# Performance work log

Measured on AMD Instinct MI355X. Metric: run time of the kernel, lower is better.

Reference implementation:

```python
import jax, jax.numpy as jnp
import numpy as np

B, L, H = 4, 512, 768          # batch, seq_len, bert hidden
S, R = 100, 100                # num candidate spans, num relation pairs
E = 128                        # size embedding dim
TE, TR = 8, 6                  # entity / relation types
MAX_ENT_LEN = 100
NEG = -1e20


def _span_masks(rng, b, n, seq_len, max_len):
    # contiguous span masks with lengths in [1, max_len-1] so sum(-1) < max_len
    starts = rng.integers(0, seq_len - 1, size=(b, n))
    lengths = rng.integers(1, max_len, size=(b, n))
    ends = np.minimum(starts + lengths, seq_len)
    pos = np.arange(seq_len)
    m = (pos[None, None, :] >= starts[..., None]) & (pos[None, None, :] < ends[..., None])
    return jnp.asarray(m.astype(np.int32))


def setup_inputs() -> dict:
    rng = np.random.default_rng(0)
    key = jax.random.key(0)
    k = jax.random.split(key, 6)
    return {
        "last_hidden_state": jax.random.normal(k[0], (B, L, H), jnp.float32),
        "entity_mask": _span_masks(rng, B, S, L, MAX_ENT_LEN),
        "relations": jnp.asarray(rng.integers(0, S, size=(B, R, 2)).astype(np.int32)),
        "relation_context_mask": _span_masks(rng, B, R, L, MAX_ENT_LEN),
        "relation_sample_mask": jnp.asarray(rng.integers(0, 2, size=(B, R)).astype(np.int32)),
        "size_emb": jax.random.normal(k[1], (MAX_ENT_LEN, E), jnp.float32) * 0.02,
        "span_w": jax.random.normal(k[2], (E + 2 * H, TE), jnp.float32) * 0.02,
        "span_b": jnp.zeros((TE,), jnp.float32),
        "rel_w": jax.random.normal(k[3], (2 * E + 3 * H, TR), jnp.float32) * 0.02,
        "rel_b": jnp.zeros((TR,), jnp.float32),
    }


def _masked_max(h, mask):
    # h: [B,L,H], mask: [B,N,L] int {0,1} -> [B,N,H]
    mf = mask[..., None].astype(h.dtype)                       # [B,N,L,1]
    masked = jnp.where(mf == 0, jnp.asarray(NEG, h.dtype), h[:, None] * mf)
    return masked.max(axis=2)


def reference(last_hidden_state, entity_mask, relations, relation_context_mask,
              relation_sample_mask, size_emb, span_w, span_b, rel_w, rel_b):
    b = last_hidden_state.shape[0]
    # ---- entity classification ----
    context = last_hidden_state[:, 0]                          # CLS pooling [B,H]
    entity_size = size_emb[entity_mask.sum(-1)]                # [B,S,E]
    entity = _masked_max(last_hidden_state, entity_mask)       # [B,S,H]
    ctx = jnp.broadcast_to(context[:, None], (b, entity.shape[1], context.shape[-1]))
    entity_repr = jnp.concatenate([entity, ctx, entity_size], axis=-1)
    entity_logit = entity_repr @ span_w + span_b               # [B,S,TE]
    # ---- relation classification ----
    rel_ctx = _masked_max(last_hidden_state, relation_context_mask)  # [B,R,H]
    rel_ctx = jnp.where(relation_sample_mask[..., None] == 1,
                        jnp.zeros((), rel_ctx.dtype), rel_ctx)
    r = relations.shape[1]
    flat = relations.reshape(b, r * 2)                         # [B,2R]
    pair = jnp.take_along_axis(entity, flat[..., None], axis=1).reshape(b, r, -1)      # [B,R,2H]
    pair_size = jnp.take_along_axis(entity_size, flat[..., None], axis=1).reshape(b, r, -1)  # [B,R,2E]
    relation_repr = jnp.concatenate([rel_ctx, pair, pair_size], axis=-1)
    relation_logit = relation_repr @ rel_w + rel_b             # [B,R,TR]
    return entity_logit, relation_logit
```

## Files before the change

kernel.cpp:

```cpp
#include <hip/hip_runtime.h>

#define Bn 4
#define Ln 512
#define Hn 768
#define Sn 100
#define Rn 100
#define En 128
#define TEn 8
#define TRn 6
#define NEGF (-1e20f)
#define W 8
#define NBLK (Ln / W)
#define H4 (Hn / 4)
#define E4 (En / 4)
#define NTHR 640

__device__ __forceinline__ float4 fmax4(float4 a, float4 b) {
    return make_float4(fmaxf(a.x, b.x), fmaxf(a.y, b.y),
                       fmaxf(a.z, b.z), fmaxf(a.w, b.w));
}

__global__ void __launch_bounds__(192)
blockmax_kernel(const float* __restrict__ hid, float* __restrict__ bmax) {
    int bj = blockIdx.x;
    int b = bj / NBLK, j = bj % NBLK;
    int tid = threadIdx.x;
    const float4* src = (const float4*)(hid + ((size_t)b * Ln + j * W) * Hn);
    float4 m0 = src[tid];
    float4 m1 = src[(size_t)H4 + tid];
    #pragma unroll
    for (int r = 2; r < W; r += 2) {
        m0 = fmax4(m0, src[(size_t)r * H4 + tid]);
        m1 = fmax4(m1, src[(size_t)(r + 1) * H4 + tid]);
    }
    ((float4*)(bmax + (size_t)bj * Hn))[tid] = fmax4(m0, m1);
}

__device__ __forceinline__ void scan_span(const int* __restrict__ mask,
                                          int lane, int* start, int* end) {
    const int4* m4 = (const int4*)(mask + lane * 8);
    int4 a = m4[0], c = m4[1];
    int mm[8] = {a.x, a.y, a.z, a.w, c.x, c.y, c.z, c.w};
    int first = 0x7fffffff, last = -1;
    #pragma unroll
    for (int r = 0; r < 8; ++r) {
        if (mm[r] != 0) {
            int row = lane * 8 + r;
            first = min(first, row);
            last = max(last, row);
        }
    }
    #pragma unroll
    for (int off = 1; off < 64; off <<= 1) {
        first = min(first, __shfl_xor(first, off, 64));
        last = max(last, __shfl_xor(last, off, 64));
    }
    *start = first;
    *end = last + 1;
}

__device__ __forceinline__ float4 span_max(const float4* __restrict__ hb4,
                                           const float4* __restrict__ bm4,
                                           int start, int end) {
    float4 m0 = make_float4(NEGF, NEGF, NEGF, NEGF);
    float4 m1 = m0;
    int jstart = (start + 7) >> 3, jend = end >> 3;
    if (jstart >= jend) {
        int r = start;
        for (; r + 2 <= end; r += 2) {
            m0 = fmax4(m0, hb4[(size_t)r * H4]);
            m1 = fmax4(m1, hb4[(size_t)(r + 1) * H4]);
        }
        if (r < end) m0 = fmax4(m0, hb4[(size_t)r * H4]);
        return fmax4(m0, m1);
    }
    int j = jstart;
    for (; j + 4 <= jend; j += 4) {
        m0 = fmax4(m0, fmax4(bm4[(size_t)j * H4], bm4[(size_t)(j + 1) * H4]));
        m1 = fmax4(m1, fmax4(bm4[(size_t)(j + 2) * H4], bm4[(size_t)(j + 3) * H4]));
    }
    for (; j < jend; ++j) m0 = fmax4(m0, bm4[(size_t)j * H4]);
    int he = jstart * W;
    int r = start;
    for (; r + 2 <= he; r += 2) {
        m0 = fmax4(m0, hb4[(size_t)r * H4]);
        m1 = fmax4(m1, hb4[(size_t)(r + 1) * H4]);
    }
    if (r < he) m0 = fmax4(m0, hb4[(size_t)r * H4]);
    r = jend * W;
    for (; r + 2 <= end; r += 2) {
        m0 = fmax4(m0, hb4[(size_t)r * H4]);
        m1 = fmax4(m1, hb4[(size_t)(r + 1) * H4]);
    }
    if (r < end) m0 = fmax4(m0, hb4[(size_t)r * H4]);
    return fmax4(m0, m1);
}

template <int NT>
__device__ __forceinline__ void dot4(const float4 v, const float* __restrict__ wbase,
                                     int row, float* acc) {
    const float* vp = &v.x;
    #pragma unroll
    for (int j = 0; j < 4; ++j) {
        const float* wr = wbase + (size_t)(4 * row + j) * NT;
        #pragma unroll
        for (int t = 0; t < NT; ++t) acc[t] += vp[j] * wr[t];
    }
}

__global__ void __launch_bounds__(NTHR)
logits_kernel(const float* __restrict__ hid,
              const int* __restrict__ ent_mask,
              const int* __restrict__ rel_mask,
              const int* __restrict__ samp_mask,
              const int* __restrict__ relations,
              const float* __restrict__ size_emb,
              const float* __restrict__ span_w,
              const float* __restrict__ span_b,
              const float* __restrict__ rel_w,
              const float* __restrict__ rel_b,
              const float* __restrict__ bmax,
              float* __restrict__ out_ent,
              float* __restrict__ out_rel) {
    int blk = blockIdx.x;
    int tid = threadIdx.x;
    int lane = tid & 63, wv = tid >> 6;

    __shared__ int se[3][2];
    __shared__ float red[10][TEn];

    float acc[TEn];
    #pragma unroll
    for (int t = 0; t < TEn; ++t) acc[t] = 0.0f;

    if (blk < Bn * Sn) {
        int b = blk / Sn;
        if (wv == 0) {
            int s0, e0;
            scan_span(ent_mask + (size_t)blk * Ln, lane, &s0, &e0);
            if (lane == 0) { se[0][0] = s0; se[0][1] = e0; }
        }
        __syncthreads();
        int start = se[0][0], end = se[0][1];
        int cnt = end - start;

        const float4* hb4 = (const float4*)(hid + (size_t)b * Ln * Hn);
        if (tid < 192) {
            const float4* bm4 = (const float4*)(bmax + (size_t)b * NBLK * Hn) + tid;
            float4 m = span_max(hb4 + tid, bm4, start, end);
            dot4<TEn>(m, span_w, tid, acc);
        } else if (tid < 384) {
            int u = tid - 192;
            dot4<TEn>(hb4[u], span_w, H4 + u, acc);
        } else if (tid < 384 + E4) {
            int u = tid - 384;
            float4 sv = ((const float4*)(size_emb + (size_t)cnt * En))[u];
            dot4<TEn>(sv, span_w, 2 * H4 + u, acc);
        }

        #pragma unroll
        for (int t = 0; t < TEn; ++t)
            #pragma unroll
            for (int off = 32; off > 0; off >>= 1)
                acc[t] += __shfl_down(acc[t], off, 64);
        if (lane == 0) {
            #pragma unroll
            for (int t = 0; t < TEn; ++t) red[wv][t] = acc[t];
        }
        __syncthreads();
        if (tid < TEn) {
            float s = span_b[tid];
            #pragma unroll
            for (int w = 0; w < 10; ++w) s += red[w][tid];
            out_ent[(size_t)blk * TEn + tid] = s;
        }
    } else {
        int rblk = blk - Bn * Sn;
        int b = rblk / Rn;
        int a0 = relations[rblk * 2 + 0];
        int a1 = relations[rblk * 2 + 1];
        bool samp = (samp_mask[rblk] == 1);

        if (wv == 0) {
            if (!samp) {
                int s0, e0;
                scan_span(rel_mask + (size_t)rblk * Ln, lane, &s0, &e0);
                if (lane == 0) { se[0][0] = s0; se[0][1] = e0; }
            }
        } else if (wv == 1) {
            int s1, e1;
            scan_span(ent_mask + ((size_t)b * Sn + a0) * Ln, lane, &s1, &e1);
            if (lane == 0) { se[1][0] = s1; se[1][1] = e1; }
        } else if (wv == 2) {
            int s2, e2;
            scan_span(ent_mask + ((size_t)b * Sn + a1) * Ln, lane, &s2, &e2);
            if (lane == 0) { se[2][0] = s2; se[2][1] = e2; }
        }
        __syncthreads();
        int cnt0 = se[1][1] - se[1][0];
        int cnt1 = se[2][1] - se[2][0];

        const float4* hb4 = (const float4*)(hid + (size_t)b * Ln * Hn);
        const float4* bm4 = (const float4*)(bmax + (size_t)b * NBLK * Hn);
        if (tid < 192) {
            if (!samp) {
                float4 m = span_max(hb4 + tid, bm4 + tid, se[0][0], se[0][1]);
                dot4<TRn>(m, rel_w, tid, acc);
            }
        } else if (tid < 384) {
            int u = tid - 192;
            float4 m = span_max(hb4 + u, bm4 + u, se[1][0], se[1][1]);
            dot4<TRn>(m, rel_w, H4 + u, acc);
        } else if (tid < 576) {
            int u = tid - 384;
            float4 m = span_max(hb4 + u, bm4 + u, se[2][0], se[2][1]);
            dot4<TRn>(m, rel_w, 2 * H4 + u, acc);
        } else if (tid < 576 + E4) {
            int u = tid - 576;
            float4 sv = ((const float4*)(size_emb + (size_t)cnt0 * En))[u];
            dot4<TRn>(sv, rel_w, 3 * H4 + u, acc);
        } else {
            int u = tid - 576 - E4;
            float4 sv = ((const float4*)(size_emb + (size_t)cnt1 * En))[u];
            dot4<TRn>(sv, rel_w, 3 * H4 + E4 + u, acc);
        }

        #pragma unroll
        for (int t = 0; t < TRn; ++t)
            #pragma unroll
            for (int off = 32; off > 0; off >>= 1)
                acc[t] += __shfl_down(acc[t], off, 64);
        if (lane == 0) {
            #pragma unroll
            for (int t = 0; t < TRn; ++t) red[wv][t] = acc[t];
        }
        __syncthreads();
        if (tid < TRn) {
            float s = rel_b[tid];
            #pragma unroll
            for (int w = 0; w < 10; ++w) s += red[w][tid];
            out_rel[(size_t)rblk * TRn + tid] = s;
        }
    }
}

extern "C" void kernel_launch(void* const* d_in, const int* in_sizes, int n_in,
                              void* d_out, int out_size, void* d_ws, size_t ws_size,
                              hipStream_t stream) {
    const float* hid       = (const float*)d_in[0];
    const int*   ent_mask  = (const int*)d_in[1];
    const int*   relations = (const int*)d_in[2];
    const int*   rel_mask  = (const int*)d_in[3];
    const int*   samp_mask = (const int*)d_in[4];
    const float* size_emb  = (const float*)d_in[5];
    const float* span_w    = (const float*)d_in[6];
    const float* span_b    = (const float*)d_in[7];
    const float* rel_w     = (const float*)d_in[8];
    const float* rel_b     = (const float*)d_in[9];

    float* out = (float*)d_out;
    float* out_ent = out;
    float* out_rel = out + Bn * Sn * TEn;

    float* bmax = (float*)d_ws;

    blockmax_kernel<<<Bn * NBLK, 192, 0, stream>>>(hid, bmax);

    logits_kernel<<<Bn * (Sn + Rn), NTHR, 0, stream>>>(
        hid, ent_mask, rel_mask, samp_mask, relations, size_emb,
        span_w, span_b, rel_w, rel_b, bmax, out_ent, out_rel);
}
```

Measured before the change: 22.25 us.

## Replace block-max prefix with sliding 16-row window max table and register weights

Swaps the 8-row block-max precompute for a per-row 16-wide sliding-window max table, so a span max becomes a few window lookups including one overlapping tail window, with no unaligned head/tail row scans. Classifier weights are also preloaded into registers as float4 vectors before the span scan, so weight loads overlap with mask scanning. The precompute now writes a full B×L×H table instead of L/8 rows, which adds write traffic and a larger workspace footprint.

```diff
diff --git a/kernel.cpp b/kernel.cpp
--- a/kernel.cpp
+++ b/kernel.cpp
@@ -9,31 +9,48 @@
 #define TEn 8
 #define TRn 6
 #define NEGF (-1e20f)
-#define W 8
-#define NBLK (Ln / W)
 #define H4 (Hn / 4)
 #define E4 (En / 4)
 #define NTHR 640
+#define WBLK 16
+#define NJ (Ln / WBLK)
+#define DCH 64
+#define NDCH (H4 / DCH)
 
 __device__ __forceinline__ float4 fmax4(float4 a, float4 b) {
     return make_float4(fmaxf(a.x, b.x), fmaxf(a.y, b.y),
                        fmaxf(a.z, b.z), fmaxf(a.w, b.w));
 }
 
-__global__ void __launch_bounds__(192)
-blockmax_kernel(const float* __restrict__ hid, float* __restrict__ bmax) {
-    int bj = blockIdx.x;
-    int b = bj / NBLK, j = bj % NBLK;
-    int tid = threadIdx.x;
-    const float4* src = (const float4*)(hid + ((size_t)b * Ln + j * W) * Hn);
-    float4 m0 = src[tid];
-    float4 m1 = src[(size_t)H4 + tid];
-    #pragma unroll
-    for (int r = 2; r < W; r += 2) {
-        m0 = fmax4(m0, src[(size_t)r * H4 + tid]);
-        m1 = fmax4(m1, src[(size_t)(r + 1) * H4 + tid]);
-    }
-    ((float4*)(bmax + (size_t)bj * Hn))[tid] = fmax4(m0, m1);
+__global__ void __launch_bounds__(64)
+win16_kernel(const float* __restrict__ hid, float* __restrict__ win) {
+    int blk = blockIdx.x;
+    int c = blk % NDCH;
+    int t = blk / NDCH;
+    int j = t % NJ, b = t / NJ;
+    int d4 = c * DCH + threadIdx.x;
+    int base = j * WBLK;
+
+    const float4* hb4 = (const float4*)(hid + (size_t)b * Ln * Hn) + d4;
+    float4 row[WBLK];
+    #pragma unroll
+    for (int k = 0; k < WBLK; ++k)
+        row[k] = hb4[(size_t)(base + k) * H4];
+    #pragma unroll
+    for (int k = WBLK - 2; k >= 0; --k)
+        row[k] = fmax4(row[k], row[k + 1]);
+
+    float4* w4 = (float4*)(win + ((size_t)b * Ln + base) * Hn) + d4;
+    w4[0] = row[0];
+    bool has_next = (j < NJ - 1);
+    float4 pre = has_next ? hb4[(size_t)(base + WBLK) * H4]
+                          : make_float4(NEGF, NEGF, NEGF, NEGF);
+    #pragma unroll
+    for (int k = 1; k < WBLK; ++k) {
+        w4[(size_t)k * H4] = fmax4(row[k], pre);
+        if (k < WBLK - 1 && has_next)
+            pre = fmax4(pre, hb4[(size_t)(base + WBLK + k) * H4]);
+    }
 }
 
 __device__ __forceinline__ void scan_span(const int* __restrict__ mask,
@@ -59,53 +76,29 @@
     *end = last + 1;
 }
 
-__device__ __forceinline__ float4 span_max(const float4* __restrict__ hb4,
-                                           const float4* __restrict__ bm4,
-                                           int start, int end) {
+__device__ __forceinline__ float4 wmax(const float4* __restrict__ hb4,
+                                       const float4* __restrict__ wn4,
+                                       int s, int e) {
     float4 m0 = make_float4(NEGF, NEGF, NEGF, NEGF);
     float4 m1 = m0;
-    int jstart = (start + 7) >> 3, jend = end >> 3;
-    if (jstart >= jend) {
-        int r = start;
-        for (; r + 2 <= end; r += 2) {
+    int cnt = e - s;
+    if (cnt >= WBLK) {
+        int r = s;
+        for (; r + 2 * WBLK <= e; r += 2 * WBLK) {
+            m0 = fmax4(m0, wn4[(size_t)r * H4]);
+            m1 = fmax4(m1, wn4[(size_t)(r + WBLK) * H4]);
+        }
+        if (r + WBLK <= e) { m0 = fmax4(m0, wn4[(size_t)r * H4]); r += WBLK; }
+        if (r < e) m1 = fmax4(m1, wn4[(size_t)(e - WBLK) * H4]);
+    } else {
+        int r = s;
+        for (; r + 2 <= e; r += 2) {
             m0 = fmax4(m0, hb4[(size_t)r * H4]);
             m1 = fmax4(m1, hb4[(size_t)(r + 1) * H4]);
         }
-        if (r < end) m0 = fmax4(m0, hb4[(size_t)r * H4]);
-        return fmax4(m0, m1);
-    }
-    int j = jstart;
-    for (; j + 4 <= jend; j += 4) {
-        m0 = fmax4(m0, fmax4(bm4[(size_t)j * H4], bm4[(size_t)(j + 1) * H4]));
-        m1 = fmax4(m1, fmax4(bm4[(size_t)(j + 2) * H4], bm4[(size_t)(j + 3) * H4]));
-    }
-    for (; j < jend; ++j) m0 = fmax4(m0, bm4[(size_t)j * H4]);
-    int he = jstart * W;
-    int r = start;
-    for (; r + 2 <= he; r += 2) {
-        m0 = fmax4(m0, hb4[(size_t)r * H4]);
-        m1 = fmax4(m1, hb4[(size_t)(r + 1) * H4]);
-    }
-    if (r < he) m0 = fmax4(m0, hb4[(size_t)r * H4]);
-    r = jend * W;
-    for (; r + 2 <= end; r += 2) {
-        m0 = fmax4(m0, hb4[(size_t)r * H4]);
-        m1 = fmax4(m1, hb4[(size_t)(r + 1) * H4]);
-    }
-    if (r < end) m0 = fmax4(m0, hb4[(size_t)r * H4]);
+        if (r < e) m0 = fmax4(m0, hb4[(size_t)r * H4]);
+    }
     return fmax4(m0, m1);
-}
-
-template <int NT>
-__device__ __forceinline__ void dot4(const float4 v, const float* __restrict__ wbase,
-                                     int row, float* acc) {
-    const float* vp = &v.x;
-    #pragma unroll
-    for (int j = 0; j < 4; ++j) {
-        const float* wr = wbase + (size_t)(4 * row + j) * NT;
-        #pragma unroll
-        for (int t = 0; t < NT; ++t) acc[t] += vp[j] * wr[t];
-    }
 }
 
 __global__ void __launch_bounds__(NTHR)
@@ -119,7 +112,7 @@
               const float* __restrict__ span_b,
               const float* __restrict__ rel_w,
               const float* __restrict__ rel_b,
-              const float* __restrict__ bmax,
+              const float* __restrict__ win,
               float* __restrict__ out_ent,
               float* __restrict__ out_rel) {
     int blk = blockIdx.x;
@@ -135,6 +128,13 @@
 
     if (blk < Bn * Sn) {
         int b = blk / Sn;
+        float w32[4 * TEn];
+        if (tid < 384 + E4) {
+            const float4* wp = (const float4*)(span_w + (size_t)tid * 4 * TEn);
+            float4* wreg = (float4*)w32;
+            #pragma unroll
+            for (int i = 0; i < TEn; ++i) wreg[i] = wp[i];
+        }
         if (wv == 0) {
             int s0, e0;
             scan_span(ent_mask + (size_t)blk * Ln, lane, &s0, &e0);
@@ -145,17 +145,25 @@
         int cnt = end - start;
 
         const float4* hb4 = (const float4*)(hid + (size_t)b * Ln * Hn);
+        const float4* wn4 = (const float4*)(win + (size_t)b * Ln * Hn);
+        float4 v = make_float4(0.f, 0.f, 0.f, 0.f);
+        bool active = true;
         if (tid < 192) {
-            const float4* bm4 = (const float4*)(bmax + (size_t)b * NBLK * Hn) + tid;
-            float4 m = span_max(hb4 + tid, bm4, start, end);
-            dot4<TEn>(m, span_w, tid, acc);
+            v = wmax(hb4 + tid, wn4 + tid, start, end);
         } else if (tid < 384) {
-            int u = tid - 192;
-            dot4<TEn>(hb4[u], span_w, H4 + u, acc);
+            v = hb4[tid - 192];
         } else if (tid < 384 + E4) {
-            int u = tid - 384;
-            float4 sv = ((const float4*)(size_emb + (size_t)cnt * En))[u];
-            dot4<TEn>(sv, span_w, 2 * H4 + u, acc);
+            v = ((const float4*)(size_emb + (size_t)cnt * En))[tid - 384];
+        } else {
+            active = false;
+        }
+        if (active) {
+            const float* vp = &v.x;
+            #pragma unroll
+            for (int j = 0; j < 4; ++j)
+                #pragma unroll
+                for (int t = 0; t < TEn; ++t)
+                    acc[t] += vp[j] * w32[j * TEn + t];
         }
 
         #pragma unroll
@@ -180,6 +188,14 @@
         int a0 = relations[rblk * 2 + 0];
         int a1 = relations[rblk * 2 + 1];
         bool samp = (samp_mask[rblk] == 1);
+
+        float w24[4 * TRn];
+        {
+            const float4* wp = (const float4*)(rel_w + (size_t)tid * 4 * TRn);
+            float4* wreg = (float4*)w24;
+            #pragma unroll
+            for (int i = 0; i < TRn; ++i) wreg[i] = wp[i];
+        }
 
         if (wv == 0) {
             if (!samp) {
@@ -201,28 +217,30 @@
         int cnt1 = se[2][1] - se[2][0];
 
         const float4* hb4 = (const float4*)(hid + (size_t)b * Ln * Hn);
-        const float4* bm4 = (const float4*)(bmax + (size_t)b * NBLK * Hn);
+        const float4* wn4 = (const float4*)(win + (size_t)b * Ln * Hn);
+        float4 v = make_float4(0.f, 0.f, 0.f, 0.f);
+        bool active = true;
         if (tid < 192) {
-            if (!samp) {
-                float4 m = span_max(hb4 + tid, bm4 + tid, se[0][0], se[0][1]);
-                dot4<TRn>(m, rel_w, tid, acc);
-            }
+            if (samp) active = false;
+            else v = wmax(hb4 + tid, wn4 + tid, se[0][0], se[0][1]);
         } else if (tid < 384) {
             int u = tid - 192;
-            float4 m = span_max(hb4 + u, bm4 + u, se[1][0], se[1][1]);
-            dot4<TRn>(m, rel_w, H4 + u, acc);
+            v = wmax(hb4 + u, wn4 + u, se[1][0], se[1][1]);
         } else if (tid < 576) {
             int u = tid - 384;
-            float4 m = span_max(hb4 + u, bm4 + u, se[2][0], se[2][1]);
-            dot4<TRn>(m, rel_w, 2 * H4 + u, acc);
+            v = wmax(hb4 + u, wn4 + u, se[2][0], se[2][1]);
         } else if (tid < 576 + E4) {
-            int u = tid - 576;
-            float4 sv = ((const float4*)(size_emb + (size_t)cnt0 * En))[u];
-            dot4<TRn>(sv, rel_w, 3 * H4 + u, acc);
+            v = ((const float4*)(size_emb + (size_t)cnt0 * En))[tid - 576];
         } else {
-            int u = tid - 576 - E4;
-            float4 sv = ((const float4*)(size_emb + (size_t)cnt1 * En))[u];
-            dot4<TRn>(sv, rel_w, 3 * H4 + E4 + u, acc);
+            v = ((const float4*)(size_emb + (size_t)cnt1 * En))[tid - 576 - E4];
+        }
+        if (active) {
+            const float* vp = &v.x;
+            #pragma unroll
+            for (int j = 0; j < 4; ++j)
+                #pragma unroll
+                for (int t = 0; t < TRn; ++t)
+                    acc[t] += vp[j] * w24[j * TRn + t];
         }
 
         #pragma unroll
@@ -262,11 +280,11 @@
     float* out_ent = out;
     float* out_rel = out + Bn * Sn * TEn;
 
-    float* bmax = (float*)d_ws;
-
-    blockmax_kernel<<<Bn * NBLK, 192, 0, stream>>>(hid, bmax);
+    float* win = (float*)d_ws;
+
+    win16_kernel<<<Bn * NJ * NDCH, 64, 0, stream>>>(hid, win);
 
     logits_kernel<<<Bn * (Sn + Rn), NTHR, 0, stream>>>(
         hid, ent_mask, rel_mask, samp_mask, relations, size_emb,
-        span_w, span_b, rel_w, rel_b, bmax, out_ent, out_rel);
-}
+        span_w, span_b, rel_w, rel_b, win, out_ent, out_rel);
+}
```

After: 23.81 us. +7.0%, slower.
